# Performance work log

Hardware: AMD Instinct MI355X
Metric: run time of the kernel (lower is better)

## Reference

```python
import jax, jax.numpy as jnp
import numpy as np
from jax import lax

EPS = 1e-5

def conv2d(x, w):
    # x: [B,C,H,W], w: [O,I,kh,kw], VALID, stride 1
    return lax.conv_general_dilated(x, w, (1, 1), 'VALID',
                                    dimension_numbers=('NCHW', 'OIHW', 'NCHW'))

def bn_eval(x, g, b, m, v):
    # per-channel eval-mode batchnorm on NCHW
    scale = g / jnp.sqrt(v + EPS)
    return x * scale[None, :, None, None] + (b - m * scale)[None, :, None, None]

def xcorr_depthwise(search, kernel):
    # search: [B,C,Hs,Ws], kernel: [B,C,hk,wk] -> [B,C,Ho,Wo]
    B, C, Hs, Ws = search.shape
    hk, wk = kernel.shape[2], kernel.shape[3]
    s = search.reshape(1, B * C, Hs, Ws)
    k = kernel.reshape(B * C, 1, hk, wk)
    out = lax.conv_general_dilated(s, k, (1, 1), 'VALID',
                                   dimension_numbers=('NCHW', 'OIHW', 'NCHW'),
                                   feature_group_count=B * C)
    return out.reshape(B, C, out.shape[2], out.shape[3])

def setup_inputs() -> dict:
    key = jax.random.key(0)
    ks = jax.random.split(key, 16)
    B, C, HID, OUT = 64, 256, 256, 10
    d = {}
    d['kernel'] = jax.random.normal(ks[0], (B, C, 7, 7), jnp.float32)
    d['search'] = jax.random.normal(ks[1], (B, C, 31, 31), jnp.float32)
    # conv_kernel branch
    d['ck_w'] = jax.random.normal(ks[2], (HID, C, 3, 3), jnp.float32) * 0.02
    d['ck_g'] = jnp.ones((HID,), jnp.float32)
    d['ck_b'] = jnp.zeros((HID,), jnp.float32)
    d['ck_m'] = jax.random.normal(ks[3], (HID,), jnp.float32) * 0.1
    d['ck_v'] = jax.random.uniform(ks[4], (HID,), jnp.float32, 0.5, 1.5)
    # conv_search branch
    d['cs_w'] = jax.random.normal(ks[5], (HID, C, 3, 3), jnp.float32) * 0.02
    d['cs_g'] = jnp.ones((HID,), jnp.float32)
    d['cs_b'] = jnp.zeros((HID,), jnp.float32)
    d['cs_m'] = jax.random.normal(ks[6], (HID,), jnp.float32) * 0.1
    d['cs_v'] = jax.random.uniform(ks[7], (HID,), jnp.float32, 0.5, 1.5)
    # head: 1x1 conv (no bias) + BN + ReLU + 1x1 conv (bias)
    d['h1_w'] = jax.random.normal(ks[8], (HID, HID), jnp.float32) * 0.05
    d['h_g'] = jnp.ones((HID,), jnp.float32)
    d['h_b'] = jnp.zeros((HID,), jnp.float32)
    d['h_m'] = jax.random.normal(ks[9], (HID,), jnp.float32) * 0.1
    d['h_v'] = jax.random.uniform(ks[10], (HID,), jnp.float32, 0.5, 1.5)
    d['h2_w'] = jax.random.normal(ks[11], (OUT, HID), jnp.float32) * 0.05
    d['h2_b'] = jnp.zeros((OUT,), jnp.float32)
    return d

def reference(kernel, search, ck_w, ck_g, ck_b, ck_m, ck_v,
              cs_w, cs_g, cs_b, cs_m, cs_v,
              h1_w, h_g, h_b, h_m, h_v, h2_w, h2_b):
    k = jax.nn.relu(bn_eval(conv2d(kernel, ck_w), ck_g, ck_b, ck_m, ck_v))   # [B,256,5,5]
    s = jax.nn.relu(bn_eval(conv2d(search, cs_w), cs_g, cs_b, cs_m, cs_v))   # [B,256,29,29]
    feat = xcorr_depthwise(s, k)                                             # [B,256,25,25]
    x = jnp.einsum('oi,bihw->bohw', h1_w, feat)
    x = jax.nn.relu(bn_eval(x, h_g, h_b, h_m, h_v))
    out = jnp.einsum('oi,bihw->bohw', h2_w, x) + h2_b[None, :, None, None]   # [B,10,25,25]
    return out
```

## Files before the change

kernel.cpp:

```cpp
#include <hip/hip_runtime.h>
#include <cstddef>
#include <cstdint>

#define BN_EPS 1e-5f

typedef __attribute__((ext_vector_type(8))) __bf16 bf16x8;
typedef __attribute__((ext_vector_type(4))) float f32x4;

__device__ inline unsigned short f2bf(float f) {
    unsigned u = __builtin_bit_cast(unsigned, f);
    unsigned r = (u + 0x7fff + ((u >> 16) & 1)) >> 16;
    return (unsigned short)r;
}
__device__ inline float bf2f(unsigned short u) {
    return __builtin_bit_cast(float, (unsigned)u << 16);
}

#define GLDS16(g, l)                                                        \
    __builtin_amdgcn_global_load_lds(                                       \
        (const __attribute__((address_space(1))) void*)(g),                 \
        (__attribute__((address_space(3))) void*)(l), 16, 0, 0)

template<int HW, int HWT>
__device__ inline void transpose_body(int rb, const float* __restrict__ in,
                                      unsigned short* __restrict__ out)
{
    __shared__ unsigned short tl[64][66];
    const int tid  = threadIdx.x;
    const int lane = tid & 63, w = tid >> 6;
    const int b  = rb / (HWT * 4);
    const int r2 = rb - b * (HWT * 4);
    const int ht = r2 >> 2, ct = r2 & 3;
    const int c0 = ct * 64, hw0 = ht * 64;
    const int hw = hw0 + lane;
    const float* ib = in + ((size_t)b * 256 + c0) * HW;
    #pragma unroll
    for (int r = 0; r < 16; ++r) {
        const int cl = w * 16 + r;
        const float v = (hw < HW) ? ib[(size_t)cl * HW + hw] : 0.f;
        tl[cl][lane] = f2bf(v);
    }
    __syncthreads();
    unsigned short* ob = out + ((size_t)b * HW + hw0) * 256 + c0 + lane;
    #pragma unroll
    for (int jj = 0; jj < 16; ++jj) {
        const int j = jj * 4 + w;
        if (hw0 + j < HW) ob[(size_t)j * 256] = tl[lane][j];
    }
}

__global__ __launch_bounds__(256)
void prep_kernel(const float* __restrict__ srch, const float* __restrict__ kin,
                 const float* __restrict__ cs_w, const float* __restrict__ ck_w,
                 const float* __restrict__ h1_w, const float* __restrict__ h2_w,
                 unsigned short* __restrict__ s16, unsigned short* __restrict__ k16,
                 unsigned short* __restrict__ wTs, unsigned short* __restrict__ wTk,
                 unsigned short* __restrict__ h1w16, unsigned short* __restrict__ h2w16,
                 int GS, int GK)
{
    const int bid = blockIdx.x;
    if (bid < GS) {
        transpose_body<961, 16>(bid, srch, s16);
    } else if (bid < GS + GK) {
        transpose_body<49, 1>(bid - GS, kin, k16);
    } else {
        const int i = (bid - GS - GK) * 256 + threadIdx.x;
        if (i < 589824) {
            const int ic = i & 255, t = i >> 8, oc = t & 255, khkw = t >> 8;
            wTs[i] = f2bf(cs_w[(size_t)((oc << 8) + ic) * 9 + khkw]);
        } else if (i < 1179648) {
            const int j = i - 589824;
            const int ic = j & 255, t = j >> 8, oc = t & 255, khkw = t >> 8;
            wTk[j] = f2bf(ck_w[(size_t)((oc << 8) + ic) * 9 + khkw]);
        } else if (i < 1245184) {
            const int j = i - 1179648;
            h1w16[j] = f2bf(h1_w[j]);
        } else if (i < 1249280) {
            const int j = i - 1245184;
            const int oc = j >> 8, ic = j & 255;
            h2w16[j] = (oc < 10) ? f2bf(h2_w[oc * 256 + ic]) : (unsigned short)0;
        }
    }
}

struct ConvParams {
    const unsigned short* bsrc;
    const unsigned short* wT;
    const float *bg, *bb, *bm, *bv;
    unsigned short* out;
    int IH, IW, OW, PPB, N;
};

__global__ __launch_bounds__(256)
void conv3x3_kernel(ConvParams S, ConvParams K, int Gs)
{
    __shared__ __align__(16) unsigned short Alds[128 * 64];
    __shared__ __align__(16) unsigned short Blds[128 * 64];

    const int tid  = threadIdx.x;
    const int lane = tid & 63;
    const int wid  = tid >> 6;

    const int raw = blockIdx.x;
    ConvParams P;
    int tileid;
    if (raw < Gs) {
        P = S;
        const int q8 = Gs >> 3, r8 = Gs & 7;
        const int xcd = raw & 7, seq = raw >> 3;
        tileid = (xcd < r8 ? xcd * (q8 + 1) : r8 * (q8 + 1) + (xcd - r8) * q8) + seq;
    } else {
        P = K;
        tileid = raw - Gs;
    }
    const int pt  = tileid >> 1;
    const int oct = tileid & 1;
    const int oc0 = oct << 7;
    const int p0  = pt << 7;

    int aoff[4], brow[4], bgs8[4], ldsrow[4];
    #pragma unroll
    for (int i = 0; i < 4; ++i) {
        const int r  = i * 32 + wid * 8 + (lane >> 3);
        const int gs = (lane & 7) ^ (r & 7);
        aoff[i] = (oc0 + r) * 256 + gs * 8;
        int pg = p0 + r; if (pg > P.N - 1) pg = P.N - 1;
        const int bb_ = pg / P.PPB;
        const int p   = pg - bb_ * P.PPB;
        const int oh  = p / P.OW, ow = p - oh * P.OW;
        brow[i] = (bb_ * P.IH + oh) * P.IW + ow;
        bgs8[i] = gs * 8;
        ldsrow[i] = (i * 32 + wid * 8) * 64;
    }

    const int q_  = lane >> 4;
    const int lr  = lane & 15;
    const int wm0 = (wid >> 1) * 64;
    const int wn0 = (wid & 1) * 64;
    const int g0  = q_ ^ (lane & 7);
    const int g1  = (4 + q_) ^ (lane & 7);
    const unsigned short* Abase = &Alds[(wm0 + lr) * 64];
    const unsigned short* Bbase = &Blds[(wn0 + lr) * 64];

    f32x4 acc[4][4] = {};

    int kh = 0, kw = 0;
    for (int khkw = 0; khkw < 9; ++khkw) {
        const size_t wslice = (size_t)khkw << 16;
        const int tapadd = kh * P.IW + kw;
        for (int ics = 0; ics < 4; ++ics) {
            const int ic0 = ics * 64;
            __syncthreads();
            #pragma unroll
            for (int i = 0; i < 4; ++i) {
                GLDS16(P.wT + wslice + aoff[i] + ic0, &Alds[ldsrow[i]]);
                GLDS16(P.bsrc + (size_t)(brow[i] + tapadd) * 256 + ic0 + bgs8[i],
                       &Blds[ldsrow[i]]);
            }
            __syncthreads();

            bf16x8 bfr[4][2];
            #pragma unroll
            for (int n = 0; n < 4; ++n) {
                bfr[n][0] = *(const bf16x8*)(Bbase + n * 1024 + g0 * 8);
                bfr[n][1] = *(const bf16x8*)(Bbase + n * 1024 + g1 * 8);
            }
            #pragma unroll
            for (int m = 0; m < 4; ++m) {
                bf16x8 a0 = *(const bf16x8*)(Abase + m * 1024 + g0 * 8);
                bf16x8 a1 = *(const bf16x8*)(Abase + m * 1024 + g1 * 8);
                #pragma unroll
                for (int n = 0; n < 4; ++n) {
                    acc[m][n] = __builtin_amdgcn_mfma_f32_16x16x32_bf16(
                                    a0, bfr[n][0], acc[m][n], 0, 0, 0);
                    acc[m][n] = __builtin_amdgcn_mfma_f32_16x16x32_bf16(
                                    a1, bfr[n][1], acc[m][n], 0, 0, 0);
                }
            }
        }
        if (++kw == 3) { kw = 0; ++kh; }
    }

    #pragma unroll
    for (int m = 0; m < 4; ++m) {
        const int ocm = oc0 + wm0 + m * 16 + q_ * 4;
        float sc[4], sh[4];
        #pragma unroll
        for (int r = 0; r < 4; ++r) {
            sc[r] = P.bg[ocm + r] * rsqrtf(P.bv[ocm + r] + BN_EPS);
            sh[r] = P.bb[ocm + r] - P.bm[ocm + r] * sc[r];
        }
        #pragma unroll
        for (int n = 0; n < 4; ++n) {
            const int pg = p0 + wn0 + n * 16 + lr;
            if (pg < P.N) {
                unsigned e0 = f2bf(fmaxf(acc[m][n][0] * sc[0] + sh[0], 0.f));
                unsigned e1 = f2bf(fmaxf(acc[m][n][1] * sc[1] + sh[1], 0.f));
                unsigned e2 = f2bf(fmaxf(acc[m][n][2] * sc[2] + sh[2], 0.f));
                unsigned e3 = f2bf(fmaxf(acc[m][n][3] * sc[3] + sh[3], 0.f));
                uint2 v; v.x = e0 | (e1 << 16); v.y = e2 | (e3 << 16);
                *(uint2*)(P.out + (size_t)pg * 256 + ocm) = v;
            }
        }
    }
}

__global__ __launch_bounds__(256)
void fused_xcorr_head_kernel(const unsigned short* __restrict__ sfeat,
                             const unsigned short* __restrict__ kfeat,
                             const unsigned short* __restrict__ h1w16,
                             const unsigned short* __restrict__ h2w16,
                             const float* __restrict__ bn_g,
                             const float* __restrict__ bn_b,
                             const float* __restrict__ bn_m,
                             const float* __restrict__ bn_v,
                             const float* __restrict__ h2b,
                             float* __restrict__ out)
{
    __shared__ __align__(16) unsigned short Alds[16384];
    __shared__ __align__(16) unsigned short Xlds[64 * 264];

    const int tid  = threadIdx.x;
    const int lane = tid & 63;
    const int wid  = tid >> 6;
    const int bid  = blockIdx.x;
    const int b    = bid / 10;
    const int pt   = bid - b * 10;
    const int p0   = pt * 64;

    {
        const int c = tid;
        float kv[25];
        const unsigned short* kp = kfeat + (size_t)b * 25 * 256 + c;
        #pragma unroll
        for (int t = 0; t < 25; ++t) kv[t] = bf2f(kp[t * 256]);

        if (pt == 9) {
            #pragma unroll
            for (int j = 49; j < 64; ++j) Xlds[j * 264 + c] = 0;
        }

        const int oh0 = p0 / 25;
        for (int ohr = 0; ohr < 4; ++ohr) {
            const int oh = oh0 + ohr;
            const int jbase = oh * 25 - p0;
            if (oh <= 24 && jbase < 64) {
                float acc[25];
                #pragma unroll
                for (int z = 0; z < 25; ++z) acc[z] = 0.f;
                const unsigned short* sp =
                    sfeat + ((size_t)(b * 29 + oh)) * 29 * 256 + c;
                #pragma unroll
                for (int i = 0; i < 5; ++i)
                    #pragma unroll
                    for (int w2 = 0; w2 < 29; ++w2) {
                        const float sv = bf2f(sp[(i * 29 + w2) * 256]);
                        #pragma unroll
                        for (int t = 0; t < 5; ++t) {
                            const int ww = w2 - t;
                            if (ww >= 0 && ww <= 24)
                                acc[ww] += sv * kv[i * 5 + t];
                        }
                    }
                #pragma unroll
                for (int ow = 0; ow < 25; ++ow) {
                    const int j = jbase + ow;
                    if (j >= 0 && j < 64)
                        Xlds[j * 264 + c] = f2bf(acc[ow]);
                }
            }
        }
    }

    const int lrow = lane >> 3;
    int aoffs[8], aldsr[8];
    #pragma unroll
    for (int s = 0; s < 8; ++s) {
        const int rowb = s * 32 + wid * 8;
        const int row  = rowb + lrow;
        const int g    = (lane & 7) ^ (row & 7);
        aoffs[s] = row * 256 + g * 8;
        aldsr[s] = rowb * 64;
    }
    const int q_ = lane >> 4;
    const int lr = lane & 15;
    const int wm = wid >> 1;
    const int wn = wid & 1;
    const int g0 = q_ ^ (lane & 7);
    const int g1 = (4 + q_) ^ (lane & 7);
    const unsigned short* Abase = &Alds[(wm * 128 + lr) * 64];

    f32x4 acc1[8][2] = {};

    for (int ics = 0; ics < 4; ++ics) {
        const int ic0 = ics * 64;
        __syncthreads();
        #pragma unroll
        for (int s = 0; s < 8; ++s)
            GLDS16(h1w16 + aoffs[s] + ic0, &Alds[aldsr[s]]);
        __syncthreads();

        bf16x8 bfr[2][2];
        #pragma unroll
        for (int n = 0; n < 2; ++n) {
            const int rowp = wn * 32 + n * 16 + lr;
            bfr[n][0] = *(const bf16x8*)(Xlds + rowp * 264 + ic0 + q_ * 8);
            bfr[n][1] = *(const bf16x8*)(Xlds + rowp * 264 + ic0 + 32 + q_ * 8);
        }
        #pragma unroll
        for (int m = 0; m < 8; ++m) {
            bf16x8 a0 = *(const bf16x8*)(Abase + m * 1024 + g0 * 8);
            bf16x8 a1 = *(const bf16x8*)(Abase + m * 1024 + g1 * 8);
            #pragma unroll
            for (int n = 0; n < 2; ++n) {
                acc1[m][n] = __builtin_amdgcn_mfma_f32_16x16x32_bf16(
                                 a0, bfr[n][0], acc1[m][n], 0, 0, 0);
                acc1[m][n] = __builtin_amdgcn_mfma_f32_16x16x32_bf16(
                                 a1, bfr[n][1], acc1[m][n], 0, 0, 0);
            }
        }
    }

    __syncthreads();
    #pragma unroll
    for (int m = 0; m < 8; ++m) {
        const int ocm = wm * 128 + m * 16 + q_ * 4;
        float sc[4], sh[4];
        #pragma unroll
        for (int r = 0; r < 4; ++r) {
            sc[r] = bn_g[ocm + r] * rsqrtf(bn_v[ocm + r] + BN_EPS);
            sh[r] = bn_b[ocm + r] - bn_m[ocm + r] * sc[r];
        }
        #pragma unroll
        for (int n = 0; n < 2; ++n) {
            const int pl = wn * 32 + n * 16 + lr;
            unsigned e0 = f2bf(fmaxf(acc1[m][n][0] * sc[0] + sh[0], 0.f));
            unsigned e1 = f2bf(fmaxf(acc1[m][n][1] * sc[1] + sh[1], 0.f));
            unsigned e2 = f2bf(fmaxf(acc1[m][n][2] * sc[2] + sh[2], 0.f));
            unsigned e3 = f2bf(fmaxf(acc1[m][n][3] * sc[3] + sh[3], 0.f));
            uint2 v; v.x = e0 | (e1 << 16); v.y = e2 | (e3 << 16);
            *(uint2*)(Xlds + (size_t)pl * 264 + ocm) = v;
        }
    }
    __syncthreads();

    const int pl = wid * 16 + lr;
    const unsigned short* arow = h2w16 + lr * 256 + q_ * 8;
    const unsigned short* brow = Xlds + (size_t)pl * 264 + q_ * 8;

    f32x4 acc2 = {};
    #pragma unroll
    for (int ks = 0; ks < 8; ++ks) {
        bf16x8 a  = *(const bf16x8*)(arow + ks * 32);
        bf16x8 bb = *(const bf16x8*)(brow + ks * 32);
        acc2 = __builtin_amdgcn_mfma_f32_16x16x32_bf16(a, bb, acc2, 0, 0, 0);
    }

    const int plocal = p0 + pl;
    if (plocal < 625) {
        #pragma unroll
        for (int r = 0; r < 4; ++r) {
            const int oc = q_ * 4 + r;
            if (oc < 10)
                out[((size_t)(b * 10 + oc)) * 625 + plocal] = acc2[r] + h2b[oc];
        }
    }
}

extern "C" void kernel_launch(void* const* d_in, const int* in_sizes, int n_in,
                              void* d_out, int out_size, void* d_ws, size_t ws_size,
                              hipStream_t stream)
{
    const float* kin  = (const float*)d_in[0];
    const float* srch = (const float*)d_in[1];
    const float* ck_w = (const float*)d_in[2];
    const float* ck_g = (const float*)d_in[3];
    const float* ck_b = (const float*)d_in[4];
    const float* ck_m = (const float*)d_in[5];
    const float* ck_v = (const float*)d_in[6];
    const float* cs_w = (const float*)d_in[7];
    const float* cs_g = (const float*)d_in[8];
    const float* cs_b = (const float*)d_in[9];
    const float* cs_m = (const float*)d_in[10];
    const float* cs_v = (const float*)d_in[11];
    const float* h1_w = (const float*)d_in[12];
    const float* h_g  = (const float*)d_in[13];
    const float* h_b  = (const float*)d_in[14];
    const float* h_m  = (const float*)d_in[15];
    const float* h_v  = (const float*)d_in[16];
    const float* h2_w = (const float*)d_in[17];
    const float* h2_b = (const float*)d_in[18];

    const int B = in_sizes[0] / (256 * 7 * 7);

    uint8_t* w = (uint8_t*)d_ws;
    unsigned short* s16     = (unsigned short*)(w);
    unsigned short* sfeat16 = (unsigned short*)(w + 31490048);
    unsigned short* kf16    = (unsigned short*)(w + 59047936);
    unsigned short* k16     = (unsigned short*)(w + 59867136);
    unsigned short* wTk     = (unsigned short*)(w + 61472768);
    unsigned short* wTs     = (unsigned short*)(w + 62652416);
    unsigned short* h1w16   = (unsigned short*)(w + 63832064);
    unsigned short* h2w16   = (unsigned short*)(w + 63963136);

    const int Ns = B * 841;
    const int Nk = B * 25;
    const int Gs = 2 * ((Ns + 127) / 128);
    const int Gk = 2 * ((Nk + 127) / 128);
    const int GS = B * 16 * 4;
    const int GK = B * 1 * 4;

    dim3 blk(256, 1, 1);

    hipLaunchKernelGGL(prep_kernel, dim3(GS + GK + 4880), blk, 0, stream,
                       srch, kin, cs_w, ck_w, h1_w, h2_w,
                       s16, k16, wTs, wTk, h1w16, h2w16, GS, GK);

    ConvParams S{ s16, wTs, cs_g, cs_b, cs_m, cs_v, sfeat16, 31, 31, 29, 841, Ns };
    ConvParams K{ k16, wTk, ck_g, ck_b, ck_m, ck_v, kf16, 7, 7, 5, 25, Nk };
    hipLaunchKernelGGL(conv3x3_kernel, dim3(Gs + Gk), blk, 0, stream, S, K, Gs);

    hipLaunchKernelGGL(fused_xcorr_head_kernel, dim3(B * 10), blk, 0, stream,
                       sfeat16, kf16, h1w16, h2w16,
                       h_g, h_b, h_m, h_v, h2_b, (float*)d_out);
}
```

Baseline: 165.3 us.

## Rewrite 3x3 conv GEMM with 256x256 tiles and double-buffered LDS pipeline

Replaces the 128x128, 4-wave conv3x3 GEMM with a 256x256 tile (all 256 output channels per block) run by 8 waves. The K loop is flattened to 36 steps over double-buffered LDS, with global-to-LDS loads for the next steps issued during MFMA phases and fenced by manual vmcnt waits, barriers and setprio. The goal is to hide load latency behind MFMA work and reuse each input tile across all output channels. In exchange the block uses 128KB of LDS and many more accumulator registers, and the grid has fewer blocks, which may lower occupancy or leave CUs idle.

```diff
diff --git a/kernel.cpp b/kernel.cpp
--- a/kernel.cpp
+++ b/kernel.cpp
@@ -91,11 +91,29 @@
     int IH, IW, OW, PPB, N;
 };
 
-__global__ __launch_bounds__(256)
-void conv3x3_kernel(ConvParams S, ConvParams K, int Gs)
+#define STAGE_A(tkt, h)                                                       \
+    { const int _b = (tkt) & 1;                                               \
+      const size_t _w = ((size_t)((tkt) >> 2) << 16) + (((tkt) & 3) << 6);    \
+      GLDS16(P.wT + _w + aoff[(h)*2],     &Alds[_b][ldsb[(h)*2]]);            \
+      GLDS16(P.wT + _w + aoff[(h)*2 + 1], &Alds[_b][ldsb[(h)*2 + 1]]); }
+
+#define STAGE_B(tkt, h)                                                       \
+    { const int _b = (tkt) & 1;                                               \
+      const int _kk = (tkt) >> 2;                                             \
+      const int _kh = _kk / 3, _kw = _kk - 3 * _kh;                           \
+      const int _tap = _kh * P.IW + _kw;                                      \
+      const int _ic = ((tkt) & 3) << 6;                                       \
+      GLDS16(P.bsrc + (size_t)(brows[(h)*2] + _tap) * 256 + _ic + gs8,        \
+             &Blds[_b][ldsb[(h)*2]]);                                         \
+      GLDS16(P.bsrc + (size_t)(brows[(h)*2+1] + _tap) * 256 + _ic + gs8,      \
+             &Blds[_b][ldsb[(h)*2+1]]); }
+
+__global__ __launch_bounds__(512, 2)
+void conv3x3_8ph_kernel(ConvParams S, ConvParams K, int Gs)
 {
-    __shared__ __align__(16) unsigned short Alds[128 * 64];
-    __shared__ __align__(16) unsigned short Blds[128 * 64];
+    constexpr int NT = 36;
+    __shared__ __align__(16) unsigned short Alds[2][256 * 64];
+    __shared__ __align__(16) unsigned short Blds[2][256 * 64];
 
     const int tid  = threadIdx.x;
     const int lane = tid & 63;
@@ -113,77 +131,92 @@
         P = K;
         tileid = raw - Gs;
     }
-    const int pt  = tileid >> 1;
-    const int oct = tileid & 1;
-    const int oc0 = oct << 7;
-    const int p0  = pt << 7;
-
-    int aoff[4], brow[4], bgs8[4], ldsrow[4];
-    #pragma unroll
-    for (int i = 0; i < 4; ++i) {
-        const int r  = i * 32 + wid * 8 + (lane >> 3);
-        const int gs = (lane & 7) ^ (r & 7);
-        aoff[i] = (oc0 + r) * 256 + gs * 8;
-        int pg = p0 + r; if (pg > P.N - 1) pg = P.N - 1;
+    const int p0 = tileid << 8;
+
+    const int gs  = (lane & 7) ^ (lane >> 3);
+    const int gs8 = gs * 8;
+    int aoff[4], brows[4], ldsb[4];
+    #pragma unroll
+    for (int s = 0; s < 4; ++s) {
+        const int rowb = (s >> 1) * 128 + (s & 1) * 64 + wid * 8;
+        const int row  = rowb + (lane >> 3);
+        aoff[s] = row * 256 + gs8;
+        int pg = p0 + row; if (pg > P.N - 1) pg = P.N - 1;
         const int bb_ = pg / P.PPB;
         const int p   = pg - bb_ * P.PPB;
         const int oh  = p / P.OW, ow = p - oh * P.OW;
-        brow[i] = (bb_ * P.IH + oh) * P.IW + ow;
-        bgs8[i] = gs * 8;
-        ldsrow[i] = (i * 32 + wid * 8) * 64;
-    }
-
-    const int q_  = lane >> 4;
-    const int lr  = lane & 15;
-    const int wm0 = (wid >> 1) * 64;
-    const int wn0 = (wid & 1) * 64;
-    const int g0  = q_ ^ (lane & 7);
-    const int g1  = (4 + q_) ^ (lane & 7);
-    const unsigned short* Abase = &Alds[(wm0 + lr) * 64];
-    const unsigned short* Bbase = &Blds[(wn0 + lr) * 64];
-
-    f32x4 acc[4][4] = {};
-
-    int kh = 0, kw = 0;
-    for (int khkw = 0; khkw < 9; ++khkw) {
-        const size_t wslice = (size_t)khkw << 16;
-        const int tapadd = kh * P.IW + kw;
-        for (int ics = 0; ics < 4; ++ics) {
-            const int ic0 = ics * 64;
-            __syncthreads();
-            #pragma unroll
-            for (int i = 0; i < 4; ++i) {
-                GLDS16(P.wT + wslice + aoff[i] + ic0, &Alds[ldsrow[i]]);
-                GLDS16(P.bsrc + (size_t)(brow[i] + tapadd) * 256 + ic0 + bgs8[i],
-                       &Blds[ldsrow[i]]);
-            }
-            __syncthreads();
-
-            bf16x8 bfr[4][2];
-            #pragma unroll
-            for (int n = 0; n < 4; ++n) {
-                bfr[n][0] = *(const bf16x8*)(Bbase + n * 1024 + g0 * 8);
-                bfr[n][1] = *(const bf16x8*)(Bbase + n * 1024 + g1 * 8);
-            }
-            #pragma unroll
-            for (int m = 0; m < 4; ++m) {
-                bf16x8 a0 = *(const bf16x8*)(Abase + m * 1024 + g0 * 8);
-                bf16x8 a1 = *(const bf16x8*)(Abase + m * 1024 + g1 * 8);
+        brows[s] = (bb_ * P.IH + oh) * P.IW + ow;
+        ldsb[s]  = rowb * 64;
+    }
+
+    const int q_ = lane >> 4;
+    const int lr = lane & 15;
+    const int x7 = lane & 7;
+    const int wm = wid >> 2;
+    const int wn = wid & 3;
+    const int g0 = (q_ ^ x7) << 3;
+    const int g1 = ((4 + q_) ^ x7) << 3;
+
+    f32x4 acc[8][4] = {};
+
+    STAGE_A(0, 0); STAGE_A(0, 1); STAGE_B(0, 0); STAGE_B(0, 1);
+    STAGE_B(1, 0); STAGE_B(1, 1);
+    asm volatile("s_waitcnt vmcnt(4)" ::: "memory");
+    __builtin_amdgcn_s_barrier();
+
+    for (int kt = 0; kt < NT; ++kt) {
+        const unsigned short* Abuf = Alds[kt & 1];
+        const unsigned short* Bbuf = Blds[kt & 1];
+        bf16x8 bfr[4][2];
+        #pragma unroll
+        for (int q = 0; q < 4; ++q) {
+            if (q == 0) {
                 #pragma unroll
                 for (int n = 0; n < 4; ++n) {
-                    acc[m][n] = __builtin_amdgcn_mfma_f32_16x16x32_bf16(
-                                    a0, bfr[n][0], acc[m][n], 0, 0, 0);
-                    acc[m][n] = __builtin_amdgcn_mfma_f32_16x16x32_bf16(
-                                    a1, bfr[n][1], acc[m][n], 0, 0, 0);
+                    const unsigned short* Bb = Bbuf + (wn * 64 + n * 16 + lr) * 64;
+                    bfr[n][0] = *(const bf16x8*)(Bb + g0);
+                    bfr[n][1] = *(const bf16x8*)(Bb + g1);
                 }
             }
-        }
-        if (++kw == 3) { kw = 0; ++kh; }
-    }
-
-    #pragma unroll
-    for (int m = 0; m < 4; ++m) {
-        const int ocm = oc0 + wm0 + m * 16 + q_ * 4;
+            bf16x8 afr[2][2];
+            #pragma unroll
+            for (int mm = 0; mm < 2; ++mm) {
+                const unsigned short* Ab =
+                    Abuf + (wm * 128 + q * 32 + mm * 16 + lr) * 64;
+                afr[mm][0] = *(const bf16x8*)(Ab + g0);
+                afr[mm][1] = *(const bf16x8*)(Ab + g1);
+            }
+            if (q == 0)      { if (kt + 1 < NT) STAGE_A(kt + 1, 0); }
+            else if (q == 1) { if (kt + 1 < NT) STAGE_A(kt + 1, 1); }
+            else if (q == 2) { if (kt + 2 < NT) STAGE_B(kt + 2, 0); }
+            else {
+                if (kt + 2 < NT) STAGE_B(kt + 2, 1);
+                if (kt + 1 < NT) {
+                    if (kt + 2 < NT) asm volatile("s_waitcnt vmcnt(4)" ::: "memory");
+                    else             asm volatile("s_waitcnt vmcnt(0)" ::: "memory");
+                }
+            }
+            __builtin_amdgcn_s_barrier();
+            asm volatile("s_waitcnt lgkmcnt(0)" ::: "memory");
+            __builtin_amdgcn_sched_barrier(0);
+            __builtin_amdgcn_s_setprio(1);
+            #pragma unroll
+            for (int mm = 0; mm < 2; ++mm)
+                #pragma unroll
+                for (int n = 0; n < 4; ++n) {
+                    acc[q * 2 + mm][n] = __builtin_amdgcn_mfma_f32_16x16x32_bf16(
+                        afr[mm][0], bfr[n][0], acc[q * 2 + mm][n], 0, 0, 0);
+                    acc[q * 2 + mm][n] = __builtin_amdgcn_mfma_f32_16x16x32_bf16(
+                        afr[mm][1], bfr[n][1], acc[q * 2 + mm][n], 0, 0, 0);
+                }
+            __builtin_amdgcn_s_setprio(0);
+            __builtin_amdgcn_s_barrier();
+        }
+    }
+
+    #pragma unroll
+    for (int m = 0; m < 8; ++m) {
+        const int ocm = wm * 128 + m * 16 + q_ * 4;
         float sc[4], sh[4];
         #pragma unroll
         for (int r = 0; r < 4; ++r) {
@@ -192,7 +225,7 @@
         }
         #pragma unroll
         for (int n = 0; n < 4; ++n) {
-            const int pg = p0 + wn0 + n * 16 + lr;
+            const int pg = p0 + wn * 64 + n * 16 + lr;
             if (pg < P.N) {
                 unsigned e0 = f2bf(fmaxf(acc[m][n][0] * sc[0] + sh[0], 0.f));
                 unsigned e1 = f2bf(fmaxf(acc[m][n][1] * sc[1] + sh[1], 0.f));
@@ -405,8 +438,8 @@
 
     const int Ns = B * 841;
     const int Nk = B * 25;
-    const int Gs = 2 * ((Ns + 127) / 128);
-    const int Gk = 2 * ((Nk + 127) / 128);
+    const int GsT = (Ns + 255) / 256;
+    const int GkT = (Nk + 255) / 256;
     const int GS = B * 16 * 4;
     const int GK = B * 1 * 4;
 
@@ -418,7 +451,8 @@
 
     ConvParams S{ s16, wTs, cs_g, cs_b, cs_m, cs_v, sfeat16, 31, 31, 29, 841, Ns };
     ConvParams K{ k16, wTk, ck_g, ck_b, ck_m, ck_v, kf16, 7, 7, 5, 25, Nk };
-    hipLaunchKernelGGL(conv3x3_kernel, dim3(Gs + Gk), blk, 0, stream, S, K, Gs);
+    hipLaunchKernelGGL(conv3x3_8ph_kernel, dim3(GsT + GkT), dim3(512, 1, 1),
+                       0, stream, S, K, GsT);
 
     hipLaunchKernelGGL(fused_xcorr_head_kernel, dim3(B * 10), blk, 0, stream,
                        sfeat16, kf16, h1w16, h2w16,
```

Result: slower. 177.1 us (+7.1%).
